# Kernel optimization log

Measured on AMD Instinct MI355X. Metric: run time of the kernel, lower is better.

The kernel has to match this reference:

```python
import jax, jax.numpy as jnp
import numpy as np

B = 1024          # batch
INPUT_LEN = 4096  # dense width of incoming activation
OUT = 4096        # out_features
FAN_IN = 128      # in_features (fixed fan-in per output)


def setup_inputs() -> dict:
    key = jax.random.key(0)
    k1, k2, k3, k4 = jax.random.split(key, 4)
    bound = 1.0 / np.sqrt(FAN_IN)
    inp = jax.random.normal(k1, (B, INPUT_LEN), dtype=jnp.float32)
    weight = jax.random.uniform(k2, (OUT, FAN_IN), dtype=jnp.float32, minval=-bound, maxval=bound)
    bias = jax.random.uniform(k3, (OUT,), dtype=jnp.float32, minval=-bound, maxval=bound)
    indx_seqs = jax.random.randint(k4, (OUT, FAN_IN), 0, INPUT_LEN, dtype=jnp.int64 if jax.config.jax_enable_x64 else jnp.int32)
    return {"input": inp, "weight": weight, "bias": bias, "indx_seqs": indx_seqs}


def reference(input, weight, bias, indx_seqs):
    # gathered: (B, OUT, FAN_IN); weight broadcast over batch; reduce fan-in.
    gathered = input[:, indx_seqs]
    out = jnp.einsum('of,bof->bo', weight, gathered) + bias
    return out
```

## Files before the change

### kernel.cpp

```cpp
#include <hip/hip_runtime.h>
#include <stdint.h>

#define NB    1024
#define IL    4096
#define NOUT  4096
#define FI    128
#define BTILE 8
#define OSPLIT 4
#define OTILE (NOUT / OSPLIT)
#define SLAB_DW (IL * (BTILE / 2))
#define SLAB_BLOCKS ((NB / BTILE) * IL / 256)
#define SORT_BLOCKS (NOUT / 4)

__device__ __forceinline__ uint32_t rne_bf16_hi(float x) {
  uint32_t u = __float_as_uint(x);
  u += 0x7FFFu + ((u >> 16) & 1u);
  return u & 0xFFFF0000u;
}

__global__ __launch_bounds__(256)
void prep_kernel(const float* __restrict__ in, uint32_t* __restrict__ slab,
                 const int* __restrict__ idx, const float* __restrict__ w,
                 uint32_t* __restrict__ pack) {
  const int bid = blockIdx.x;
  if (bid < SLAB_BLOCKS) {
    int t = bid * 256 + threadIdx.x;
    int g = t >> 12;
    int i = t & (IL - 1);
    const float* base = in + (size_t)g * (8 * IL) + i;
    uint4 v;
    v.x = rne_bf16_hi(base[1 * IL]) | (rne_bf16_hi(base[0 * IL]) >> 16);
    v.y = rne_bf16_hi(base[3 * IL]) | (rne_bf16_hi(base[2 * IL]) >> 16);
    v.z = rne_bf16_hi(base[5 * IL]) | (rne_bf16_hi(base[4 * IL]) >> 16);
    v.w = rne_bf16_hi(base[7 * IL]) | (rne_bf16_hi(base[6 * IL]) >> 16);
    reinterpret_cast<uint4*>(slab)[t] = v;
  } else {
    const int o = (bid - SLAB_BLOCKS) * 4 + (threadIdx.x >> 6);
    const unsigned lane = threadIdx.x & 63u;
    const uint32_t r = (uint32_t)(o & 7);
    const int*   irow = idx + (size_t)o * FI;
    const float* wrow = w   + (size_t)o * FI;
    uint32_t* prow = pack + (size_t)o * FI;

    uint32_t i0 = (uint32_t)irow[lane], i1 = (uint32_t)irow[64 + lane];
    uint32_t w0 = rne_bf16_hi(wrow[lane]), w1 = rne_bf16_hi(wrow[64 + lane]);
    uint32_t k0 = i0 & 7u, k1 = i1 & 7u;
    const uint64_t lt = (1ull << lane) - 1ull;

    uint32_t rank0 = 0, rank1 = 0;
    uint64_t cntp = 0;
    #pragma unroll
    for (int g = 0; g < 8; ++g) {
      uint64_t b0 = __ballot(k0 == (uint32_t)g);
      uint64_t b1 = __ballot(k1 == (uint32_t)g);
      uint32_t c0 = (uint32_t)__popcll(b0);
      if (k0 == (uint32_t)g) rank0 = (uint32_t)__popcll(b0 & lt);
      if (k1 == (uint32_t)g) rank1 = c0 + (uint32_t)__popcll(b1 & lt);
      cntp |= (uint64_t)(c0 + (uint32_t)__popcll(b1)) << (8 * g);
    }
    uint64_t ov0 = __ballot(rank0 >= 16u);
    uint64_t ov1 = __ballot(rank1 >= 16u);
    uint32_t ofr0 = (uint32_t)__popcll(ov0 & lt);
    uint32_t ofr1 = (uint32_t)__popcll(ov0) + (uint32_t)__popcll(ov1 & lt);

    auto place = [&](uint32_t k, uint32_t rank, uint32_t ofr) -> uint32_t {
      if (rank < 16u) return ((k - r) & 7u) + 8u * rank;
      uint32_t cum = 0, p = 0;
      bool done = false;
      #pragma unroll
      for (int lc = 0; lc < 8; ++lc) {
        uint32_t gl = ((uint32_t)lc + r) & 7u;
        uint32_t c  = (uint32_t)((cntp >> (8 * gl)) & 0xFFu);
        uint32_t u  = c < 16u ? c : 16u;
        uint32_t lcnt = 16u - u;
        if (!done && ofr < cum + lcnt) { p = (uint32_t)lc + 8u * (u + ofr - cum); done = true; }
        cum += lcnt;
      }
      return p;
    };
    prow[place(k0, rank0, ofr0)] = w0 | ((i0 << 4) & 0xFFFFu);
    prow[place(k1, rank1, ofr1)] = w1 | ((i1 << 4) & 0xFFFFu);
  }
}

__global__ __launch_bounds__(1024)
void lincond_kernel(const uint32_t* __restrict__ slab,
                    const uint32_t* __restrict__ pack,
                    const float* __restrict__ bias,
                    float* __restrict__ out) {
  __shared__ uint32_t lds[SLAB_DW];
  const int bid   = blockIdx.x;
  const int b0    = (bid >> 2) * BTILE;
  const int obase = (bid & 3) * OTILE;
  const int tid   = threadIdx.x;

  const uint32_t* src = slab + (size_t)(b0 >> 3) * SLAB_DW;
  #pragma unroll
  for (int r = 0; r < 4; ++r) {
    int e = (r * 1024 + tid) * 4;
    __builtin_amdgcn_global_load_lds(
        (const __attribute__((address_space(1))) uint32_t*)(src + e),
        (__attribute__((address_space(3))) uint32_t*)(lds + e),
        16, 0, 0);
  }
  __syncthreads();

  const int o = obase + tid;
  const char* ldsb = reinterpret_cast<const char*>(lds);
  float acc[8] = {0.f,0.f,0.f,0.f,0.f,0.f,0.f,0.f};
  const uint4* pw = reinterpret_cast<const uint4*>(pack) + (size_t)o * (FI / 4);

  #pragma unroll 2
  for (int j = 0; j < 8; ++j) {
    uint4 pq[4];
    #pragma unroll
    for (int q = 0; q < 4; ++q) pq[q] = pw[j * 4 + q];
    uint32_t pvw[16];
    #pragma unroll
    for (int q = 0; q < 4; ++q) {
      pvw[q * 4 + 0] = pq[q].x; pvw[q * 4 + 1] = pq[q].y;
      pvw[q * 4 + 2] = pq[q].z; pvw[q * 4 + 3] = pq[q].w;
    }
    #pragma unroll
    for (int h = 0; h < 2; ++h) {
      uint4 g[8];
      #pragma unroll
      for (int c = 0; c < 8; ++c)
        g[c] = *reinterpret_cast<const uint4*>(ldsb + (pvw[h * 8 + c] & 0xFFFFu));
      #pragma unroll
      for (int c = 0; c < 8; ++c) {
        float wv = __uint_as_float(pvw[h * 8 + c] & 0xFFFF0000u);
        acc[0] = fmaf(wv, __uint_as_float(g[c].x << 16),         acc[0]);
        acc[1] = fmaf(wv, __uint_as_float(g[c].x & 0xFFFF0000u), acc[1]);
        acc[2] = fmaf(wv, __uint_as_float(g[c].y << 16),         acc[2]);
        acc[3] = fmaf(wv, __uint_as_float(g[c].y & 0xFFFF0000u), acc[3]);
        acc[4] = fmaf(wv, __uint_as_float(g[c].z << 16),         acc[4]);
        acc[5] = fmaf(wv, __uint_as_float(g[c].z & 0xFFFF0000u), acc[5]);
        acc[6] = fmaf(wv, __uint_as_float(g[c].w << 16),         acc[6]);
        acc[7] = fmaf(wv, __uint_as_float(g[c].w & 0xFFFF0000u), acc[7]);
      }
    }
  }

  const float bv = bias[o];
  #pragma unroll
  for (int k = 0; k < 8; ++k)
    out[(size_t)(b0 + k) * NOUT + o] = acc[k] + bv;
}

__global__ __launch_bounds__(256)
void lincond_raw(const float* __restrict__ input, const float* __restrict__ wgt,
                 const float* __restrict__ bias, const int* __restrict__ idxs,
                 float* __restrict__ out) {
  int t = blockIdx.x * 256 + threadIdx.x;
  int b = t >> 12, o = t & (NOUT - 1);
  const float* irow = input + (size_t)b * IL;
  const int*   ix   = idxs + (size_t)o * FI;
  const float* wr   = wgt  + (size_t)o * FI;
  float acc = bias[o];
  for (int f = 0; f < FI; ++f) acc += wr[f] * irow[ix[f]];
  out[t] = acc;
}

extern "C" void kernel_launch(void* const* d_in, const int* in_sizes, int n_in,
                              void* d_out, int out_size, void* d_ws, size_t ws_size,
                              hipStream_t stream) {
  const float* input  = (const float*)d_in[0];
  const float* weight = (const float*)d_in[1];
  const float* bias   = (const float*)d_in[2];
  const int*   idxs   = (const int*)d_in[3];
  float*       out    = (float*)d_out;

  const size_t pack_bytes = (size_t)NOUT * FI * sizeof(uint32_t);
  const size_t slab_bytes = (size_t)(NB / BTILE) * SLAB_DW * sizeof(uint32_t);
  const int grid = (NB / BTILE) * OSPLIT;

  if (ws_size >= pack_bytes + slab_bytes) {
    uint32_t* pack = (uint32_t*)d_ws;
    uint32_t* slab = (uint32_t*)((char*)d_ws + pack_bytes);
    prep_kernel<<<SLAB_BLOCKS + SORT_BLOCKS, 256, 0, stream>>>(input, slab, idxs, weight, pack);
    lincond_kernel<<<grid, 1024, 0, stream>>>(slab, pack, bias, out);
  } else {
    lincond_raw<<<(NB * NOUT) / 256, 256, 0, stream>>>(input, weight, bias, idxs, out);
  }
}
```

Before: 55.58 us.

## Switch gathered activations and weights to fp16 and use packed fdot2 accumulation

```diff
diff --git a/kernel.cpp b/kernel.cpp
--- a/kernel.cpp
+++ b/kernel.cpp
@@ -1,4 +1,5 @@
 #include <hip/hip_runtime.h>
+#include <hip/hip_fp16.h>
 #include <stdint.h>
 
 #define NB    1024
@@ -12,16 +13,23 @@
 #define SLAB_BLOCKS ((NB / BTILE) * IL / 256)
 #define SORT_BLOCKS (NOUT / 4)
 
-__device__ __forceinline__ uint32_t rne_bf16_hi(float x) {
-  uint32_t u = __float_as_uint(x);
-  u += 0x7FFFu + ((u >> 16) & 1u);
-  return u & 0xFFFF0000u;
+typedef _Float16 h2v __attribute__((ext_vector_type(2)));
+__device__ __forceinline__ h2v as_h2(uint32_t u){ union{uint32_t u; h2v h;} c; c.u=u; return c.h; }
+#if __has_builtin(__builtin_amdgcn_fdot2)
+__device__ __forceinline__ float fdot2(h2v a, h2v b, float c){ return __builtin_amdgcn_fdot2(a,b,c,false); }
+#else
+__device__ __forceinline__ float fdot2(h2v a, h2v b, float c){ return c + (float)a[0]*(float)b[0] + (float)a[1]*(float)b[1]; }
+#endif
+
+__device__ __forceinline__ uint32_t f16bits(float x) {
+  return (uint32_t)__half_as_ushort(__float2half(x));
 }
 
 __global__ __launch_bounds__(256)
 void prep_kernel(const float* __restrict__ in, uint32_t* __restrict__ slab,
                  const int* __restrict__ idx, const float* __restrict__ w,
-                 uint32_t* __restrict__ pack) {
+                 uint2* __restrict__ pack2) {
+  __shared__ uint32_t sbuf[4][FI];
   const int bid = blockIdx.x;
   if (bid < SLAB_BLOCKS) {
     int t = bid * 256 + threadIdx.x;
@@ -29,21 +37,22 @@
     int i = t & (IL - 1);
     const float* base = in + (size_t)g * (8 * IL) + i;
     uint4 v;
-    v.x = rne_bf16_hi(base[1 * IL]) | (rne_bf16_hi(base[0 * IL]) >> 16);
-    v.y = rne_bf16_hi(base[3 * IL]) | (rne_bf16_hi(base[2 * IL]) >> 16);
-    v.z = rne_bf16_hi(base[5 * IL]) | (rne_bf16_hi(base[4 * IL]) >> 16);
-    v.w = rne_bf16_hi(base[7 * IL]) | (rne_bf16_hi(base[6 * IL]) >> 16);
+    v.x = (f16bits(base[1 * IL]) << 16) | f16bits(base[0 * IL]);
+    v.y = (f16bits(base[3 * IL]) << 16) | f16bits(base[2 * IL]);
+    v.z = (f16bits(base[5 * IL]) << 16) | f16bits(base[4 * IL]);
+    v.w = (f16bits(base[7 * IL]) << 16) | f16bits(base[6 * IL]);
     reinterpret_cast<uint4*>(slab)[t] = v;
   } else {
-    const int o = (bid - SLAB_BLOCKS) * 4 + (threadIdx.x >> 6);
+    const int wv = threadIdx.x >> 6;
+    const int o = (bid - SLAB_BLOCKS) * 4 + wv;
     const unsigned lane = threadIdx.x & 63u;
     const uint32_t r = (uint32_t)(o & 7);
     const int*   irow = idx + (size_t)o * FI;
     const float* wrow = w   + (size_t)o * FI;
-    uint32_t* prow = pack + (size_t)o * FI;
 
     uint32_t i0 = (uint32_t)irow[lane], i1 = (uint32_t)irow[64 + lane];
-    uint32_t w0 = rne_bf16_hi(wrow[lane]), w1 = rne_bf16_hi(wrow[64 + lane]);
+    uint32_t e0 = (f16bits(wrow[lane])      << 16) | ((i0 << 4) & 0xFFFFu);
+    uint32_t e1 = (f16bits(wrow[64 + lane]) << 16) | ((i1 << 4) & 0xFFFFu);
     uint32_t k0 = i0 & 7u, k1 = i1 & 7u;
     const uint64_t lt = (1ull << lane) - 1ull;
 
@@ -78,23 +87,19 @@
       }
       return p;
     };
-    prow[place(k0, rank0, ofr0)] = w0 | ((i0 << 4) & 0xFFFFu);
-    prow[place(k1, rank1, ofr1)] = w1 | ((i1 << 4) & 0xFFFFu);
+    sbuf[wv][place(k0, rank0, ofr0)] = e0;
+    sbuf[wv][place(k1, rank1, ofr1)] = e1;
+    __syncthreads();
+
+    uint32_t s0 = sbuf[wv][2 * lane], s1 = sbuf[wv][2 * lane + 1];
+    uint2 pe;
+    pe.x = ((s0 & 0xFFFFu) << 16) | (s1 & 0xFFFFu);
+    pe.y = (s1 & 0xFFFF0000u) | (s0 >> 16);
+    pack2[(size_t)o * 64 + lane] = pe;
   }
 }
 
-__global__ __launch_bounds__(1024)
-void lincond_kernel(const uint32_t* __restrict__ slab,
-                    const uint32_t* __restrict__ pack,
-                    const float* __restrict__ bias,
-                    float* __restrict__ out) {
-  __shared__ uint32_t lds[SLAB_DW];
-  const int bid   = blockIdx.x;
-  const int b0    = (bid >> 2) * BTILE;
-  const int obase = (bid & 3) * OTILE;
-  const int tid   = threadIdx.x;
-
-  const uint32_t* src = slab + (size_t)(b0 >> 3) * SLAB_DW;
+__device__ __forceinline__ void stage_slab(const uint32_t* src, uint32_t* lds, int tid) {
   #pragma unroll
   for (int r = 0; r < 4; ++r) {
     int e = (r * 1024 + tid) * 4;
@@ -103,42 +108,50 @@
         (__attribute__((address_space(3))) uint32_t*)(lds + e),
         16, 0, 0);
   }
+}
+
+__global__ __launch_bounds__(1024)
+void lincond_kernel(const uint32_t* __restrict__ slab,
+                    const uint2* __restrict__ pack2,
+                    const float* __restrict__ bias,
+                    float* __restrict__ out) {
+  __shared__ uint32_t lds[SLAB_DW];
+  const int bid   = blockIdx.x;
+  const int b0    = (bid >> 2) * BTILE;
+  const int obase = (bid & 3) * OTILE;
+  const int tid   = threadIdx.x;
+  stage_slab(slab + (size_t)(b0 >> 3) * SLAB_DW, lds, tid);
   __syncthreads();
 
   const int o = obase + tid;
   const char* ldsb = reinterpret_cast<const char*>(lds);
   float acc[8] = {0.f,0.f,0.f,0.f,0.f,0.f,0.f,0.f};
-  const uint4* pw = reinterpret_cast<const uint4*>(pack) + (size_t)o * (FI / 4);
+  const uint4* pw4 = reinterpret_cast<const uint4*>(pack2) + (size_t)o * 32;
+
+#define DOT2P(U1, U2, WT, K0, K1) {                                             \
+    acc[K0] = fdot2(as_h2(__builtin_amdgcn_perm((U2), (U1), 0x05040100u)),      \
+                    as_h2(WT), acc[K0]);                                        \
+    acc[K1] = fdot2(as_h2(__builtin_amdgcn_perm((U2), (U1), 0x07060302u)),      \
+                    as_h2(WT), acc[K1]);}
+
+#define ENTRY(AD, WT) {                                                         \
+    uint32_t a1 = (AD) >> 16, a2 = (AD) & 0xFFFFu;                              \
+    uint4 g1 = *reinterpret_cast<const uint4*>(ldsb + a1);                      \
+    uint4 g2 = *reinterpret_cast<const uint4*>(ldsb + a2);                      \
+    DOT2P(g1.x, g2.x, WT, 0, 1)                                                 \
+    DOT2P(g1.y, g2.y, WT, 2, 3)                                                 \
+    DOT2P(g1.z, g2.z, WT, 4, 5)                                                 \
+    DOT2P(g1.w, g2.w, WT, 6, 7)}
 
   #pragma unroll 2
   for (int j = 0; j < 8; ++j) {
     uint4 pq[4];
     #pragma unroll
-    for (int q = 0; q < 4; ++q) pq[q] = pw[j * 4 + q];
-    uint32_t pvw[16];
+    for (int q = 0; q < 4; ++q) pq[q] = pw4[j * 4 + q];
     #pragma unroll
     for (int q = 0; q < 4; ++q) {
-      pvw[q * 4 + 0] = pq[q].x; pvw[q * 4 + 1] = pq[q].y;
-      pvw[q * 4 + 2] = pq[q].z; pvw[q * 4 + 3] = pq[q].w;
-    }
-    #pragma unroll
-    for (int h = 0; h < 2; ++h) {
-      uint4 g[8];
-      #pragma unroll
-      for (int c = 0; c < 8; ++c)
-        g[c] = *reinterpret_cast<const uint4*>(ldsb + (pvw[h * 8 + c] & 0xFFFFu));
-      #pragma unroll
-      for (int c = 0; c < 8; ++c) {
-        float wv = __uint_as_float(pvw[h * 8 + c] & 0xFFFF0000u);
-        acc[0] = fmaf(wv, __uint_as_float(g[c].x << 16),         acc[0]);
-        acc[1] = fmaf(wv, __uint_as_float(g[c].x & 0xFFFF0000u), acc[1]);
-        acc[2] = fmaf(wv, __uint_as_float(g[c].y << 16),         acc[2]);
-        acc[3] = fmaf(wv, __uint_as_float(g[c].y & 0xFFFF0000u), acc[3]);
-        acc[4] = fmaf(wv, __uint_as_float(g[c].z << 16),         acc[4]);
-        acc[5] = fmaf(wv, __uint_as_float(g[c].z & 0xFFFF0000u), acc[5]);
-        acc[6] = fmaf(wv, __uint_as_float(g[c].w << 16),         acc[6]);
-        acc[7] = fmaf(wv, __uint_as_float(g[c].w & 0xFFFF0000u), acc[7]);
-      }
+      ENTRY(pq[q].x, pq[q].y)
+      ENTRY(pq[q].z, pq[q].w)
     }
   }
 
@@ -171,15 +184,15 @@
   const int*   idxs   = (const int*)d_in[3];
   float*       out    = (float*)d_out;
 
-  const size_t pack_bytes = (size_t)NOUT * FI * sizeof(uint32_t);
+  const size_t pack_bytes = (size_t)NOUT * 64 * sizeof(uint2);
   const size_t slab_bytes = (size_t)(NB / BTILE) * SLAB_DW * sizeof(uint32_t);
   const int grid = (NB / BTILE) * OSPLIT;
 
   if (ws_size >= pack_bytes + slab_bytes) {
-    uint32_t* pack = (uint32_t*)d_ws;
-    uint32_t* slab = (uint32_t*)((char*)d_ws + pack_bytes);
-    prep_kernel<<<SLAB_BLOCKS + SORT_BLOCKS, 256, 0, stream>>>(input, slab, idxs, weight, pack);
-    lincond_kernel<<<grid, 1024, 0, stream>>>(slab, pack, bias, out);
+    uint2*    pack2 = (uint2*)d_ws;
+    uint32_t* slab  = (uint32_t*)((char*)d_ws + pack_bytes);
+    prep_kernel<<<SLAB_BLOCKS + SORT_BLOCKS, 256, 0, stream>>>(input, slab, idxs, weight, pack2);
+    lincond_kernel<<<grid, 1024, 0, stream>>>(slab, pack2, bias, out);
   } else {
     lincond_raw<<<(NB * NOUT) / 256, 256, 0, stream>>>(input, weight, bias, idxs, out);
   }
```

Result: faster. 52.94 us (-4.7%).
